# Performance work log

Hardware: AMD Instinct MI355X
Metric: run time of the kernel (lower is better)

Reference implementation:

```python
import jax, jax.numpy as jnp
import numpy as np

N, E, D_IN, H, C = 100000, 1600000, 256, 128, 10


def setup_inputs() -> dict:
    key = jax.random.key(0)
    ks = jax.random.split(key, 12)
    x = jax.random.normal(ks[0], (N, D_IN), dtype=jnp.float32)
    edge_index = jax.random.randint(ks[1], (2, E), 0, N, dtype=jnp.int64)
    reranker_scores = jax.random.normal(ks[2], (N,), dtype=jnp.float32)
    s_in = 1.0 / np.sqrt(D_IN)
    s_h = 1.0 / np.sqrt(H)
    # SAGEConv: lin_l applies to aggregated neighbors (with bias), lin_r to root (no bias)
    W_l = jax.random.uniform(ks[3], (H, D_IN), jnp.float32, -s_in, s_in)
    b_l = jax.random.uniform(ks[4], (H,), jnp.float32, -s_in, s_in)
    W_r = jax.random.uniform(ks[5], (H, D_IN), jnp.float32, -s_in, s_in)
    W_res = jax.random.uniform(ks[6], (H, D_IN), jnp.float32, -s_in, s_in)
    b_res = jax.random.uniform(ks[7], (H,), jnp.float32, -s_in, s_in)
    W_score = jax.random.uniform(ks[8], (1, H), jnp.float32, -s_h, s_h)
    b_score = jax.random.uniform(ks[9], (1,), jnp.float32, -s_h, s_h)
    W_crit = jax.random.uniform(ks[10], (C, H), jnp.float32, -s_h, s_h)
    b_crit = jax.random.uniform(ks[11], (C,), jnp.float32, -s_h, s_h)
    alpha = jnp.float32(0.65)
    return {"x": x, "edge_index": edge_index, "reranker_scores": reranker_scores,
            "W_l": W_l, "b_l": b_l, "W_r": W_r, "W_res": W_res, "b_res": b_res,
            "W_score": W_score, "b_score": b_score, "W_crit": W_crit, "b_crit": b_crit,
            "alpha": alpha}


def reference(x, edge_index, reranker_scores, W_l, b_l, W_r, W_res, b_res,
              W_score, b_score, W_crit, b_crit, alpha):
    src, dst = edge_index[0], edge_index[1]
    n = x.shape[0]
    ones = jnp.ones(src.shape[0], dtype=x.dtype)
    deg = jax.ops.segment_sum(ones, dst, num_segments=n)          # [N]
    nbr_sum = jax.ops.segment_sum(x[src], dst, num_segments=n)    # [N, D_IN]
    agg = nbr_sum / jnp.maximum(deg, 1.0)[:, None]                # mean aggregation
    # SAGEConv: lin_l(agg) + lin_r(x); relu; dropout (eval -> identity); residual
    h = jax.nn.relu(agg @ W_l.T + b_l + x @ W_r.T)                # [N, H]
    h = h + (x @ W_res.T + b_res)                                 # residual projection
    gnn_scores = (h @ W_score.T + b_score)[:, 0]                  # [N]
    a = jax.nn.sigmoid(alpha)
    final_scores = a * reranker_scores + (1.0 - a) * gnn_scores
    criterion_logits = h @ W_crit.T + b_crit                      # [N, C]
    return final_scores, criterion_logits
```

## Files before the change

kernel.cpp:

```cpp
#include <hip/hip_runtime.h>
#include <math.h>

#define DIN 256
#define HDIM 128
#define NCRIT 10
#define BSH 9
#define EPB 4096

typedef __bf16 bf16;
typedef bf16 bf16x8 __attribute__((ext_vector_type(8)));
typedef float f32x4 __attribute__((ext_vector_type(4)));
typedef float f32x2 __attribute__((ext_vector_type(2)));

static inline size_t alignup(size_t x, size_t a) { return (x + a - 1) & ~(a - 1); }

__device__ inline float bflo(unsigned v) { return __uint_as_float(v << 16); }
__device__ inline float bfhi(unsigned v) { return __uint_as_float(v & 0xffff0000u); }

__device__ inline bf16x8 cvt8(float4 v0, float4 v1) {
    bf16x8 w;
    w[0] = (bf16)v0.x; w[1] = (bf16)v0.y; w[2] = (bf16)v0.z; w[3] = (bf16)v0.w;
    w[4] = (bf16)v1.x; w[5] = (bf16)v1.y; w[6] = (bf16)v1.z; w[7] = (bf16)v1.w;
    return w;
}

__device__ inline void gl_lds16(const void* g, void* l) {
    __builtin_amdgcn_global_load_lds(
        (const __attribute__((address_space(1))) unsigned*)g,
        (__attribute__((address_space(3))) unsigned*)l, 16, 0, 0);
}

__global__ __launch_bounds__(256) void k_bucket2(
    const int* __restrict__ src, const int* __restrict__ dst, int E,
    int* __restrict__ bcnt, int2* __restrict__ bpool, int capb, int nB,
    const float* __restrict__ Wl, const float* __restrict__ Wr,
    const float* __restrict__ Wres,
    const float* __restrict__ wscore, const float* __restrict__ wcrit,
    const float* __restrict__ bres, const float* __restrict__ bscore,
    const float* __restrict__ bcrit,
    bf16* __restrict__ WcatT, float* __restrict__ cq)
{
    int t = threadIdx.x;
    int b = blockIdx.x;
    if (b < 64) {
        int base = (b * 256 + t) * 4;
        int r = base >> 8;
        int c0 = base & 255;
        const float* W = (r < 128) ? Wl : Wr;
        float4 v = *(const float4*)&W[(size_t)(r & 127) * 256 + c0];
        bf16 o[4] = {(bf16)v.x, (bf16)v.y, (bf16)v.z, (bf16)v.w};
        char* d = (char*)WcatT + ((((size_t)(c0 >> 3) * 272 + r) << 4) + ((c0 & 7) << 1));
        *(uint2*)d = *(const uint2*)o;
        return;
    } else if (b < 80) {
        int q = b - 64;
        int k = t;
        float s = 0.f;
        if (q < 11) {
            const float* wepi = (q == 0) ? wscore : &wcrit[(size_t)(q - 1) * HDIM];
            for (int c = 0; c < HDIM; ++c)
                s += wepi[c] * Wres[(size_t)c * 256 + k];
        }
        char* d = (char*)WcatT + ((((size_t)(k >> 3) * 272 + 256 + q) << 4) + ((k & 7) << 1));
        *(bf16*)d = (bf16)s;
        return;
    } else if (b == 80) {
        if (t < 11) {
            const float* wepi = (t == 0) ? wscore : &wcrit[(size_t)(t - 1) * HDIM];
            float s = 0.f;
            for (int c = 0; c < HDIM; ++c) s += bres[c] * wepi[c];
            cq[t] = s + ((t == 0) ? bscore[0] : bcrit[t - 1]);
        }
        return;
    }

    __shared__ int lcnt[256], lbase[256], lcur[256], gbase[256];
    __shared__ int2 stage[EPB];

    int blk = b - 81;
    int base = blk * EPB;
    int m = min(EPB, E - base);
    if (m <= 0) return;

    lcnt[t] = 0;
    __syncthreads();
    for (int i = t; i < m; i += 256)
        atomicAdd(&lcnt[dst[base + i] >> BSH], 1);
    __syncthreads();
    int c0 = lcnt[t];
    for (int d = 1; d < 256; d <<= 1) {
        int a0 = lcnt[t];
        int b0 = (t >= d) ? lcnt[t - d] : 0;
        __syncthreads();
        lcnt[t] = a0 + b0;
        __syncthreads();
    }
    int e0 = lcnt[t] - c0;
    lbase[t] = e0;
    lcur[t] = e0;
    if (t < nB && c0 > 0) gbase[t] = atomicAdd(&bcnt[t * 16], c0);
    __syncthreads();
    for (int i = t; i < m; i += 256) {
        int s2 = src[base + i], d = dst[base + i];
        int bk = d >> BSH;
        int pos = atomicAdd(&lcur[bk], 1);
        stage[pos] = make_int2(s2, d);
    }
    __syncthreads();
    int wv = t >> 6, lane = t & 63;
    for (int bk = wv; bk < nB; bk += 4) {
        int lb = lbase[bk];
        int cb = lcnt[bk] - lb;
        if (cb == 0) continue;
        int gb = gbase[bk];
        int2* dstp = bpool + (size_t)bk * capb + gb;
        for (int j = lane; j < cb && gb + j < capb; j += 64)
            dstp[j] = stage[lb + j];
    }
}

__global__ __launch_bounds__(256) void k_fin(const int* __restrict__ bcnt,
                                             const int2* __restrict__ bpool, int capb,
                                             int n, int* __restrict__ off,
                                             int* __restrict__ cnt, int* __restrict__ sidx) {
    __shared__ int lcnt[512], lcur[512];
    int b = blockIdx.x, t = threadIdx.x;
    int m = min(bcnt[b * 16], capb);
    const int2* ep = bpool + (size_t)b * capb;

    lcnt[t] = 0; lcnt[t + 256] = 0;
    __syncthreads();
    for (int i = t; i < m; i += 256) {
        int2 e = ep[i];
        atomicAdd(&lcnt[e.y & 511], 1);
    }
    __syncthreads();
    int c0 = lcnt[t], c1 = lcnt[t + 256];
    for (int d = 1; d < 512; d <<= 1) {
        int a0 = lcnt[t], a1 = lcnt[t + 256];
        int b0 = (t >= d) ? lcnt[t - d] : 0;
        int b1 = ((t + 256) >= d) ? lcnt[t + 256 - d] : 0;
        __syncthreads();
        lcnt[t] = a0 + b0; lcnt[t + 256] = a1 + b1;
        __syncthreads();
    }
    int e0 = lcnt[t] - c0, e1 = lcnt[t + 256] - c1;
    int nbase = b << BSH;
    int sbase = b * capb;
    lcur[t] = e0; lcur[t + 256] = e1;
    int n0 = nbase + t, n1 = nbase + t + 256;
    if (n0 < n) { off[n0] = sbase + e0; cnt[n0] = c0; }
    if (n1 < n) { off[n1] = sbase + e1; cnt[n1] = c1; }
    __syncthreads();
    for (int i = t; i < m; i += 256) {
        int2 e = ep[i];
        int pos = atomicAdd(&lcur[e.y & 511], 1);
        sidx[sbase + pos] = e.x;
    }
}

__global__ __launch_bounds__(512) void k_gemm(
    const float* __restrict__ x, const bf16* __restrict__ WcatT, int n,
    unsigned char* __restrict__ yq, bf16* __restrict__ z, float* __restrict__ w,
    const float* __restrict__ bl)
{
    __shared__ __align__(16) char smem[147456];
    int t = threadIdx.x;
    int wv = t >> 6, lane = t & 63;
    int l15 = lane & 15, kq = lane >> 4;

    {
        int cbase0 = wv * 64;
        #pragma unroll
        for (int i = 0; i < 17; i++) {
            int cbase = i * 512 + cbase0;
            gl_lds16((const char*)WcatT + (((size_t)cbase + lane) << 4),
                     smem + ((size_t)cbase << 4));
        }
    }
    __syncthreads();

    char* scr = smem + 139264 + wv * 1024;
    int rrow = lane >> 2, rc4 = (lane & 3) * 4;

    int nTiles = (n + 127) >> 7;
    for (int tile = blockIdx.x; tile < nTiles; tile += gridDim.x) {
        int rowb = tile * 128 + wv * 16;
        int myrow = rowb + l15;
        const float* ap = x + (size_t)(myrow < n ? myrow : (n - 1)) * 256 + kq * 8;

        float4 xa[8], xb[8];
        #pragma unroll
        for (int s = 0; s < 8; s++) {
            xa[s] = *(const float4*)(ap + s * 32);
            xb[s] = *(const float4*)(ap + s * 32 + 4);
        }

        f32x4 acc[17];
        #pragma unroll
        for (int C = 0; C < 17; C++) acc[C] = (f32x4){0.f, 0.f, 0.f, 0.f};

        #pragma unroll
        for (int s = 0; s < 8; s++) {
            bf16x8 afr = cvt8(xa[s], xb[s]);
            int sbase = ((s * 4 + kq) * 272 + l15) << 4;
            #pragma unroll
            for (int C = 0; C < 17; C++) {
                bf16x8 b = *(const bf16x8*)(smem + sbase + C * 256);
                acc[C] = __builtin_amdgcn_mfma_f32_16x16x32_bf16(afr, b, acc[C], 0, 0, 0);
            }
        }

        int gr = rowb + rrow;
        bool ok = gr < n;
        #pragma unroll
        for (int C = 0; C < 17; C++) {
            #pragma unroll
            for (int j = 0; j < 4; j++)
                *(float*)(scr + ((((kq << 2) + j) * 16 + l15) << 2)) = acc[C][j];
            f32x4 vv = *(const f32x4*)(scr + ((rrow * 16 + rc4) << 2));
            if (C < 8) {
                unsigned pk = (unsigned)__builtin_amdgcn_cvt_pk_fp8_f32(vv[0], vv[1], 0, false);
                pk = (unsigned)__builtin_amdgcn_cvt_pk_fp8_f32(vv[2], vv[3], pk, true);
                if (ok) *(unsigned*)(yq + (size_t)gr * 128 + C * 16 + rc4) = pk;
            } else if (C < 16) {
                float4 blv = *(const float4*)&bl[(C - 8) * 16 + rc4];
                bf16 o[4] = {(bf16)(vv[0] + blv.x), (bf16)(vv[1] + blv.y),
                             (bf16)(vv[2] + blv.z), (bf16)(vv[3] + blv.w)};
                if (ok) *(uint2*)((char*)z + (size_t)gr * 256 + (C - 8) * 32 + rc4 * 2) =
                            *(const uint2*)o;
            } else {
                if (ok) *(f32x4*)(w + (size_t)gr * 16 + rc4) = vv;
            }
        }
    }
}

__global__ __launch_bounds__(256) void k_gather(
    const unsigned char* __restrict__ yq, const bf16* __restrict__ z,
    const float* __restrict__ w, const float* __restrict__ cq,
    const int* __restrict__ off, const int* __restrict__ cnt, const int* __restrict__ sidx,
    const float* __restrict__ wscore, const float* __restrict__ wcrit,
    const float* __restrict__ rrs, const float* __restrict__ palpha,
    int n, float* __restrict__ outF, float* __restrict__ outL)
{
    __shared__ bf16 wsb[11 * 128];
    int t = threadIdx.x;
    for (int i = t; i < 11 * 128; i += 256) {
        int q = i >> 7, c = i & 127;
        wsb[i] = (bf16)((q == 0) ? wscore[c] : wcrit[(size_t)(q - 1) * HDIM + c]);
    }
    __syncthreads();

    int node = blockIdx.x * 4 + (t >> 6);
    if (node >= n) return;
    int lane = t & 63, g4 = lane >> 4, c16 = lane & 15;

    uint4 zv = *(const uint4*)((const char*)z + (size_t)node * 256 + c16 * 16);

    const unsigned char* ybase = yq + c16 * 8;
    int beg = off[node], len = cnt[node];
    const int* sp = sidx + beg;

    f32x2 a01 = {0.f, 0.f}, a23 = {0.f, 0.f}, a45 = {0.f, 0.f}, a67 = {0.f, 0.f};
    int e = 0;
    for (; e + 8 <= len; e += 8) {
        int i0 = sp[e + g4];
        int i1 = sp[e + 4 + g4];
        uint2 v0 = *(const uint2*)(ybase + ((size_t)(unsigned)i0 << 7));
        uint2 v1 = *(const uint2*)(ybase + ((size_t)(unsigned)i1 << 7));
        a01 += __builtin_amdgcn_cvt_pk_f32_fp8(v0.x, false)
             + __builtin_amdgcn_cvt_pk_f32_fp8(v1.x, false);
        a23 += __builtin_amdgcn_cvt_pk_f32_fp8(v0.x, true)
             + __builtin_amdgcn_cvt_pk_f32_fp8(v1.x, true);
        a45 += __builtin_amdgcn_cvt_pk_f32_fp8(v0.y, false)
             + __builtin_amdgcn_cvt_pk_f32_fp8(v1.y, false);
        a67 += __builtin_amdgcn_cvt_pk_f32_fp8(v0.y, true)
             + __builtin_amdgcn_cvt_pk_f32_fp8(v1.y, true);
    }
    for (; e < len; e += 4) {
        int slot = e + g4;
        int ii = sp[slot < len ? slot : len - 1];
        uint2 v = *(const uint2*)(ybase + ((size_t)(unsigned)ii << 7));
        if (slot < len) {
            a01 += __builtin_amdgcn_cvt_pk_f32_fp8(v.x, false);
            a23 += __builtin_amdgcn_cvt_pk_f32_fp8(v.x, true);
            a45 += __builtin_amdgcn_cvt_pk_f32_fp8(v.y, false);
            a67 += __builtin_amdgcn_cvt_pk_f32_fp8(v.y, true);
        }
    }
    float a[8] = {a01[0], a01[1], a23[0], a23[1], a45[0], a45[1], a67[0], a67[1]};
    #pragma unroll
    for (int j = 0; j < 8; j++) {
        a[j] += __shfl_xor(a[j], 16, 64);
        a[j] += __shfl_xor(a[j], 32, 64);
    }
    float inv = 1.f / fmaxf((float)len, 1.f);

    float zf[8] = {bflo(zv.x), bfhi(zv.x), bflo(zv.y), bfhi(zv.y),
                   bflo(zv.z), bfhi(zv.z), bflo(zv.w), bfhi(zv.w)};
    float h[8];
    #pragma unroll
    for (int j = 0; j < 8; j++)
        h[j] = fmaxf(a[j] * inv + zf[j], 0.f);

    float p[3];
    #pragma unroll
    for (int qq = 0; qq < 3; qq++) {
        int q = g4 * 3 + qq;
        float s = 0.f;
        if (q < 11) {
            uint4 ww = *(const uint4*)&wsb[q * 128 + c16 * 8];
            s = h[0] * bflo(ww.x) + h[1] * bfhi(ww.x)
              + h[2] * bflo(ww.y) + h[3] * bfhi(ww.y)
              + h[4] * bflo(ww.z) + h[5] * bfhi(ww.z)
              + h[6] * bflo(ww.w) + h[7] * bfhi(ww.w);
        }
        #pragma unroll
        for (int d = 1; d < 16; d <<= 1)
            s += __shfl_xor(s, d, 64);
        p[qq] = s;
    }
    if (c16 == 0) {
        #pragma unroll
        for (int qq = 0; qq < 3; qq++) {
            int q = g4 * 3 + qq;
            if (q >= 11) continue;
            float val = p[qq] + w[(size_t)node * 16 + q] + cq[q];
            if (q == 0) {
                float al = palpha[0];
                float aa = 1.f / (1.f + expf(-al));
                outF[node] = aa * rrs[node] + (1.f - aa) * val;
            } else {
                outL[(size_t)node * NCRIT + q - 1] = val;
            }
        }
    }
}

extern "C" void kernel_launch(void* const* d_in, const int* in_sizes, int n_in,
                              void* d_out, int out_size, void* d_ws, size_t ws_size,
                              hipStream_t stream) {
    const float* x      = (const float*)d_in[0];
    const int*   ei     = (const int*)d_in[1];
    const float* rrs    = (const float*)d_in[2];
    const float* Wl     = (const float*)d_in[3];
    const float* bl     = (const float*)d_in[4];
    const float* Wr     = (const float*)d_in[5];
    const float* Wres   = (const float*)d_in[6];
    const float* bres   = (const float*)d_in[7];
    const float* wscore = (const float*)d_in[8];
    const float* bscore = (const float*)d_in[9];
    const float* wcrit  = (const float*)d_in[10];
    const float* bcrit  = (const float*)d_in[11];
    const float* alpha  = (const float*)d_in[12];

    int N = in_sizes[0] / DIN;
    int E = in_sizes[1] / 2;
    const int* srcv = ei;
    const int* dstv = ei + E;

    int nB = (N + 511) >> BSH;
    int capb = (E / (nB > 0 ? nB : 1)) * 2 + 256;

    char* p = (char*)d_ws;
    int* bcnt  = (int*)p; p += alignup((size_t)nB * 16 * 4, 256);
    int2* bpool = (int2*)p; p += alignup((size_t)nB * capb * 8, 256);
    int* off   = (int*)p; p += alignup((size_t)N * 4, 256);
    int* cnt   = (int*)p; p += alignup((size_t)N * 4, 256);
    int* sidx  = (int*)p; p += alignup((size_t)nB * capb * 4, 256);
    bf16* WcatT = (bf16*)p; p += alignup((size_t)32 * 272 * 16, 256);
    unsigned char* yq = (unsigned char*)p; p += alignup((size_t)N * HDIM, 256);
    bf16* z    = (bf16*)p; p += alignup((size_t)N * HDIM * 2, 256);
    float* w   = (float*)p; p += alignup((size_t)N * 16 * 4, 256);
    float* cq  = (float*)p; p += 256;

    hipMemsetAsync(bcnt, 0, (size_t)nB * 16 * 4, stream);

    k_bucket2<<<81 + (E + EPB - 1) / EPB, 256, 0, stream>>>(
        srcv, dstv, E, bcnt, bpool, capb, nB, Wl, Wr, Wres, wscore, wcrit,
        bres, bscore, bcrit, WcatT, cq);
    k_fin<<<nB, 256, 0, stream>>>(bcnt, bpool, capb, N, off, cnt, sidx);

    k_gemm<<<256, 512, 0, stream>>>(x, WcatT, N, yq, z, w, bl);

    float* outF = (float*)d_out;
    float* outL = outF + N;
    k_gather<<<(N + 3) / 4, 256, 0, stream>>>(yq, z, w, cq, off, cnt, sidx,
                                              wscore, wcrit, rrs, alpha, N, outF, outL);
}
```

Before: 185.6 us.

## Partition fp8 neighbor features into column slabs and split gather from epilogue

The GEMM now writes the fp8 projected neighbor features in eight column-partitioned slabs of 16 bytes per node instead of row-major 128-byte rows. A new partitioned gather kernel reduces each slab separately, with the slab index taken from blockIdx low bits, so each pass touches a smaller footprint that can stay in cache. It writes mean-aggregated bf16 results to a new buffer that a separate epilogue kernel reads. This adds a kernel launch and an extra N×128 bf16 write and read round trip. It also adds an intermediate bf16 rounding of the aggregate and re-reads the edge index list eight times.

```diff
diff --git a/kernel.cpp b/kernel.cpp
--- a/kernel.cpp
+++ b/kernel.cpp
@@ -161,7 +161,7 @@
 
 __global__ __launch_bounds__(512) void k_gemm(
     const float* __restrict__ x, const bf16* __restrict__ WcatT, int n,
-    unsigned char* __restrict__ yq, bf16* __restrict__ z, float* __restrict__ w,
+    unsigned char* __restrict__ yp, bf16* __restrict__ z, float* __restrict__ w,
     const float* __restrict__ bl)
 {
     __shared__ __align__(16) char smem[147456];
@@ -222,7 +222,7 @@
             if (C < 8) {
                 unsigned pk = (unsigned)__builtin_amdgcn_cvt_pk_fp8_f32(vv[0], vv[1], 0, false);
                 pk = (unsigned)__builtin_amdgcn_cvt_pk_fp8_f32(vv[2], vv[3], pk, true);
-                if (ok) *(unsigned*)(yq + (size_t)gr * 128 + C * 16 + rc4) = pk;
+                if (ok) *(unsigned*)(yp + (((size_t)C * n + gr) << 4) + rc4) = pk;
             } else if (C < 16) {
                 float4 blv = *(const float4*)&bl[(C - 8) * 16 + rc4];
                 bf16 o[4] = {(bf16)(vv[0] + blv.x), (bf16)(vv[1] + blv.y),
@@ -236,10 +236,51 @@
     }
 }
 
-__global__ __launch_bounds__(256) void k_gather(
-    const unsigned char* __restrict__ yq, const bf16* __restrict__ z,
+__global__ __launch_bounds__(512) void k_pgather(
+    const unsigned char* __restrict__ yp,
+    const int* __restrict__ off, const int* __restrict__ cnt, const int* __restrict__ sidx,
+    int n, bf16* __restrict__ aggy)
+{
+    int bid = blockIdx.x;
+    int p = bid & 7;
+    int nodeblk = bid >> 3;
+    int t = threadIdx.x;
+    int node = nodeblk * 8 + (t >> 6);
+    if (node >= n) return;
+    int lane = t & 63, e4 = lane >> 2, c4 = lane & 3;
+
+    const unsigned char* ybase = yp + (((size_t)p * n) << 4) + c4 * 4;
+    int beg = off[node], len = cnt[node];
+    const int* sp = sidx + beg;
+
+    f32x2 a01 = {0.f, 0.f}, a23 = {0.f, 0.f};
+    for (int e = 0; e < len; e += 16) {
+        int slot = e + e4;
+        int ii = sp[slot < len ? slot : len - 1];
+        int v = *(const int*)(ybase + ((size_t)(unsigned)ii << 4));
+        if (slot < len) {
+            a01 += __builtin_amdgcn_cvt_pk_f32_fp8(v, false);
+            a23 += __builtin_amdgcn_cvt_pk_f32_fp8(v, true);
+        }
+    }
+    #pragma unroll
+    for (int d = 4; d < 64; d <<= 1) {
+        a01[0] += __shfl_xor(a01[0], d, 64);
+        a01[1] += __shfl_xor(a01[1], d, 64);
+        a23[0] += __shfl_xor(a23[0], d, 64);
+        a23[1] += __shfl_xor(a23[1], d, 64);
+    }
+    if (e4 == 0) {
+        float inv = 1.f / fmaxf((float)len, 1.f);
+        bf16 o[4] = {(bf16)(a01[0] * inv), (bf16)(a01[1] * inv),
+                     (bf16)(a23[0] * inv), (bf16)(a23[1] * inv)};
+        *(uint2*)((char*)aggy + (((size_t)p * n + node) << 5) + c4 * 8) = *(const uint2*)o;
+    }
+}
+
+__global__ __launch_bounds__(256) void k_epi(
+    const bf16* __restrict__ aggy, const bf16* __restrict__ z,
     const float* __restrict__ w, const float* __restrict__ cq,
-    const int* __restrict__ off, const int* __restrict__ cnt, const int* __restrict__ sidx,
     const float* __restrict__ wscore, const float* __restrict__ wcrit,
     const float* __restrict__ rrs, const float* __restrict__ palpha,
     int n, float* __restrict__ outF, float* __restrict__ outL)
@@ -256,53 +297,18 @@
     if (node >= n) return;
     int lane = t & 63, g4 = lane >> 4, c16 = lane & 15;
 
+    uint4 av = *(const uint4*)((const char*)aggy
+                   + (((size_t)(c16 >> 1) * n + node) << 5) + (c16 & 1) * 16);
     uint4 zv = *(const uint4*)((const char*)z + (size_t)node * 256 + c16 * 16);
 
-    const unsigned char* ybase = yq + c16 * 8;
-    int beg = off[node], len = cnt[node];
-    const int* sp = sidx + beg;
-
-    f32x2 a01 = {0.f, 0.f}, a23 = {0.f, 0.f}, a45 = {0.f, 0.f}, a67 = {0.f, 0.f};
-    int e = 0;
-    for (; e + 8 <= len; e += 8) {
-        int i0 = sp[e + g4];
-        int i1 = sp[e + 4 + g4];
-        uint2 v0 = *(const uint2*)(ybase + ((size_t)(unsigned)i0 << 7));
-        uint2 v1 = *(const uint2*)(ybase + ((size_t)(unsigned)i1 << 7));
-        a01 += __builtin_amdgcn_cvt_pk_f32_fp8(v0.x, false)
-             + __builtin_amdgcn_cvt_pk_f32_fp8(v1.x, false);
-        a23 += __builtin_amdgcn_cvt_pk_f32_fp8(v0.x, true)
-             + __builtin_amdgcn_cvt_pk_f32_fp8(v1.x, true);
-        a45 += __builtin_amdgcn_cvt_pk_f32_fp8(v0.y, false)
-             + __builtin_amdgcn_cvt_pk_f32_fp8(v1.y, false);
-        a67 += __builtin_amdgcn_cvt_pk_f32_fp8(v0.y, true)
-             + __builtin_amdgcn_cvt_pk_f32_fp8(v1.y, true);
-    }
-    for (; e < len; e += 4) {
-        int slot = e + g4;
-        int ii = sp[slot < len ? slot : len - 1];
-        uint2 v = *(const uint2*)(ybase + ((size_t)(unsigned)ii << 7));
-        if (slot < len) {
-            a01 += __builtin_amdgcn_cvt_pk_f32_fp8(v.x, false);
-            a23 += __builtin_amdgcn_cvt_pk_f32_fp8(v.x, true);
-            a45 += __builtin_amdgcn_cvt_pk_f32_fp8(v.y, false);
-            a67 += __builtin_amdgcn_cvt_pk_f32_fp8(v.y, true);
-        }
-    }
-    float a[8] = {a01[0], a01[1], a23[0], a23[1], a45[0], a45[1], a67[0], a67[1]};
-    #pragma unroll
-    for (int j = 0; j < 8; j++) {
-        a[j] += __shfl_xor(a[j], 16, 64);
-        a[j] += __shfl_xor(a[j], 32, 64);
-    }
-    float inv = 1.f / fmaxf((float)len, 1.f);
-
+    float af[8] = {bflo(av.x), bfhi(av.x), bflo(av.y), bfhi(av.y),
+                   bflo(av.z), bfhi(av.z), bflo(av.w), bfhi(av.w)};
     float zf[8] = {bflo(zv.x), bfhi(zv.x), bflo(zv.y), bfhi(zv.y),
                    bflo(zv.z), bfhi(zv.z), bflo(zv.w), bfhi(zv.w)};
     float h[8];
     #pragma unroll
     for (int j = 0; j < 8; j++)
-        h[j] = fmaxf(a[j] * inv + zf[j], 0.f);
+        h[j] = fmaxf(af[j] + zf[j], 0.f);
 
     float p[3];
     #pragma unroll
@@ -370,10 +376,11 @@
     int* cnt   = (int*)p; p += alignup((size_t)N * 4, 256);
     int* sidx  = (int*)p; p += alignup((size_t)nB * capb * 4, 256);
     bf16* WcatT = (bf16*)p; p += alignup((size_t)32 * 272 * 16, 256);
-    unsigned char* yq = (unsigned char*)p; p += alignup((size_t)N * HDIM, 256);
+    unsigned char* yp = (unsigned char*)p; p += alignup((size_t)N * HDIM, 256);
     bf16* z    = (bf16*)p; p += alignup((size_t)N * HDIM * 2, 256);
     float* w   = (float*)p; p += alignup((size_t)N * 16 * 4, 256);
     float* cq  = (float*)p; p += 256;
+    bf16* aggy = (bf16*)p; p += alignup((size_t)N * HDIM * 2, 256);
 
     hipMemsetAsync(bcnt, 0, (size_t)nB * 16 * 4, stream);
 
@@ -382,10 +389,13 @@
         bres, bscore, bcrit, WcatT, cq);
     k_fin<<<nB, 256, 0, stream>>>(bcnt, bpool, capb, N, off, cnt, sidx);
 
-    k_gemm<<<256, 512, 0, stream>>>(x, WcatT, N, yq, z, w, bl);
+    k_gemm<<<256, 512, 0, stream>>>(x, WcatT, N, yp, z, w, bl);
+
+    int nodeblks = (N + 7) / 8;
+    k_pgather<<<nodeblks * 8, 512, 0, stream>>>(yp, off, cnt, sidx, N, aggy);
 
     float* outF = (float*)d_out;
     float* outL = outF + N;
-    k_gather<<<(N + 3) / 4, 256, 0, stream>>>(yq, z, w, cq, off, cnt, sidx,
-                                              wscore, wcrit, rrs, alpha, N, outF, outL);
-}
+    k_epi<<<(N + 3) / 4, 256, 0, stream>>>(aggy, z, w, cq, wscore, wcrit,
+                                           rrs, alpha, N, outF, outL);
+}
```

After: 347.0 us. 87.0% more time.

## Pad per-node CSR segments to 4 entries and gather with int4 index loads

Applied to the files above, without the earlier changes.

Per-node edge segments in the bucketed CSR are now padded to a multiple of 4 and the per-bucket capacity is rounded to 4 and enlarged, so each node's index list starts 16-byte aligned. The aggregation kernel gets a new 16-edge unrolled loop in which each 16-lane group loads four neighbour indices with one int4 load and issues four fp8 row gathers. This is meant to cut index-load instructions and raise memory-level parallelism in the gather. The cost is a larger scratch buffer, an extra pair of LDS barriers in the scan kernel, and higher register use in the aggregation kernel.

```diff
diff --git a/kernel.cpp b/kernel.cpp
--- a/kernel.cpp
+++ b/kernel.cpp
@@ -136,6 +136,10 @@
     }
     __syncthreads();
     int c0 = lcnt[t], c1 = lcnt[t + 256];
+    int p0 = (c0 + 3) & ~3, p1 = (c1 + 3) & ~3;
+    __syncthreads();
+    lcnt[t] = p0; lcnt[t + 256] = p1;
+    __syncthreads();
     for (int d = 1; d < 512; d <<= 1) {
         int a0 = lcnt[t], a1 = lcnt[t + 256];
         int b0 = (t >= d) ? lcnt[t - d] : 0;
@@ -144,7 +148,7 @@
         lcnt[t] = a0 + b0; lcnt[t + 256] = a1 + b1;
         __syncthreads();
     }
-    int e0 = lcnt[t] - c0, e1 = lcnt[t + 256] - c1;
+    int e0 = lcnt[t] - p0, e1 = lcnt[t + 256] - p1;
     int nbase = b << BSH;
     int sbase = b * capb;
     lcur[t] = e0; lcur[t + 256] = e1;
@@ -264,6 +268,29 @@
 
     f32x2 a01 = {0.f, 0.f}, a23 = {0.f, 0.f}, a45 = {0.f, 0.f}, a67 = {0.f, 0.f};
     int e = 0;
+    for (; e + 16 <= len; e += 16) {
+        int4 iv = *(const int4*)&sp[e + g4 * 4];
+        uint2 v0 = *(const uint2*)(ybase + ((size_t)(unsigned)iv.x << 7));
+        uint2 v1 = *(const uint2*)(ybase + ((size_t)(unsigned)iv.y << 7));
+        uint2 v2 = *(const uint2*)(ybase + ((size_t)(unsigned)iv.z << 7));
+        uint2 v3 = *(const uint2*)(ybase + ((size_t)(unsigned)iv.w << 7));
+        a01 += __builtin_amdgcn_cvt_pk_f32_fp8(v0.x, false)
+             + __builtin_amdgcn_cvt_pk_f32_fp8(v1.x, false)
+             + __builtin_amdgcn_cvt_pk_f32_fp8(v2.x, false)
+             + __builtin_amdgcn_cvt_pk_f32_fp8(v3.x, false);
+        a23 += __builtin_amdgcn_cvt_pk_f32_fp8(v0.x, true)
+             + __builtin_amdgcn_cvt_pk_f32_fp8(v1.x, true)
+             + __builtin_amdgcn_cvt_pk_f32_fp8(v2.x, true)
+             + __builtin_amdgcn_cvt_pk_f32_fp8(v3.x, true);
+        a45 += __builtin_amdgcn_cvt_pk_f32_fp8(v0.y, false)
+             + __builtin_amdgcn_cvt_pk_f32_fp8(v1.y, false)
+             + __builtin_amdgcn_cvt_pk_f32_fp8(v2.y, false)
+             + __builtin_amdgcn_cvt_pk_f32_fp8(v3.y, false);
+        a67 += __builtin_amdgcn_cvt_pk_f32_fp8(v0.y, true)
+             + __builtin_amdgcn_cvt_pk_f32_fp8(v1.y, true)
+             + __builtin_amdgcn_cvt_pk_f32_fp8(v2.y, true)
+             + __builtin_amdgcn_cvt_pk_f32_fp8(v3.y, true);
+    }
     for (; e + 8 <= len; e += 8) {
         int i0 = sp[e + g4];
         int i1 = sp[e + 4 + g4];
@@ -361,7 +388,7 @@
     const int* dstv = ei + E;
 
     int nB = (N + 511) >> BSH;
-    int capb = (E / (nB > 0 ? nB : 1)) * 2 + 256;
+    int capb = (int)alignup((size_t)(E / (nB > 0 ? nB : 1)) * 2 + 256 + 2048, 4);
 
     char* p = (char*)d_ws;
     int* bcnt  = (int*)p; p += alignup((size_t)nB * 16 * 4, 256);
```

New measurement: 180.1 us. 1.03x faster.
